# Performance work log

Measured on AMD Instinct MI355X. Metric: run time of the kernel, lower is better.

## Reference

```python
import jax, jax.numpy as jnp
import numpy as np

IN_F, OUT_F = 512, 512
GRID_SIZE, SPLINE_ORDER = 5, 3
K = GRID_SIZE + SPLINE_ORDER  # 8 basis functions
B, S = 8, 1024


def setup_inputs() -> dict:
    key = jax.random.key(0)
    k1, k2, k3, k4, k5 = jax.random.split(key, 5)
    return {
        "x": jax.random.normal(k1, (B, S, IN_F), dtype=jnp.float32),
        "coeff": jax.random.normal(k2, (OUT_F, IN_F, K), dtype=jnp.float32),
        "scale_base": jax.random.normal(k3, (OUT_F, IN_F), dtype=jnp.float32) * 0.1,
        "scale_spline": jax.random.normal(k4, (OUT_F, IN_F), dtype=jnp.float32),
        "base_bias": jax.random.normal(k5, (OUT_F, IN_F), dtype=jnp.float32),
    }


def reference(x, coeff, scale_base, scale_spline, base_bias):
    batch = x.shape[0]
    in_f = x.shape[-1]
    k = coeff.shape[-1]

    xc = jnp.clip(x.reshape(-1, in_f), -1.0, 1.0)      # (N, in)
    base = jax.nn.silu(xc)                              # (N, in)

    # polynomial basis recurrence: b0 = 1, b1 = x, b_i = 2*x*b_{i-1} - 1
    bases = [jnp.ones_like(xc), xc]
    for _ in range(2, k):
        bases.append(2.0 * xc * bases[-1] - 1.0)
    basis = jnp.stack(bases[:k], axis=-1)               # (N, in, K)

    # spline[n,o] = sum_{i,k} scale_spline[o,i]*coeff[o,i,k]*basis[n,i,k]
    w_spline = scale_spline[..., None] * coeff          # (out, in, K)
    spline_term = jnp.einsum('nik,oik->no', basis, w_spline)
    base_term = base @ scale_base.T                     # (N, out)
    out = base_term + spline_term + jnp.sum(base_bias, axis=1)  # (N, out)

    out = out.reshape(batch, -1, base_bias.shape[0])    # (B, S, out)
    if out.shape[-2] == 1:
        out = out[..., 0, :]
    return out
```

## Files before the change

### kernel.cpp

```cpp
#include <hip/hip_runtime.h>
#include <hip/hip_bf16.h>

#define IN_FEAT 512
#define OUT_FEAT 512
#define NTOK 8192
#define KDIM 4096

typedef short bf16x8 __attribute__((ext_vector_type(8)));
typedef float f32x16 __attribute__((ext_vector_type(16)));

static __device__ inline short f2bf(float f) {
    union { float f; unsigned u; } v; v.f = f;
    unsigned u = v.u;
    u += 0x7fffu + ((u >> 16) & 1u);
    return (short)(u >> 16);
}

static __device__ inline unsigned pack2bf(float f0, float f1) {
    union { float f; unsigned u; } a, b; a.f = f0; b.f = f1;
    return __builtin_amdgcn_perm(b.u + 0x8000u, a.u + 0x8000u, 0x07060302u);
}

static __device__ inline bf16x8 gen_chunk(float xv) {
    float xc = fminf(fmaxf(xv, -1.f), 1.f);
    float e  = __expf(-xc);
    float bse = xc * __builtin_amdgcn_rcpf(1.f + e);
    float b2 = 2.f * xc * xc - 1.f;
    float b3 = 2.f * xc * b2 - 1.f;
    float b4 = 2.f * xc * b3 - 1.f;
    float b5 = 2.f * xc * b4 - 1.f;
    float b6 = 2.f * xc * b5 - 1.f;
    float b7 = 2.f * xc * b6 - 1.f;
    union { uint4 u; bf16x8 v; } r;
    r.u.x = pack2bf(bse, xc);
    r.u.y = pack2bf(b2, b3);
    r.u.z = pack2bf(b4, b5);
    r.u.w = pack2bf(b6, b7);
    return r.v;
}

static __device__ inline void gload_lds16(const short* g, short* l) {
    __builtin_amdgcn_global_load_lds(
        (const __attribute__((address_space(1))) unsigned int*)g,
        (__attribute__((address_space(3))) unsigned int*)l,
        16, 0, 0);
}

__global__ __launch_bounds__(256) void kan_prep(
    const float* __restrict__ coeff, const float* __restrict__ scale_base,
    const float* __restrict__ scale_spline, const float* __restrict__ base_bias,
    short* __restrict__ Wb, float* __restrict__ bias)
{
    int o = blockIdx.x;
    int tid = threadIdx.x;
    float local = 0.f;
#pragma unroll
    for (int rep = 0; rep < 2; ++rep) {
        int i = tid + rep * 256;
        size_t oi = (size_t)o * IN_FEAT + i;
        const float4* c4 = (const float4*)(coeff + oi * 8);
        float4 ca = c4[0], cb = c4[1];
        float ss = scale_spline[oi];
        float sb = scale_base[oi];
        local += base_bias[oi] + ss * ca.x;
        bf16x8 w;
        w[0] = f2bf(sb);
        w[1] = f2bf(ss * ca.y); w[2] = f2bf(ss * ca.z); w[3] = f2bf(ss * ca.w);
        w[4] = f2bf(ss * cb.x); w[5] = f2bf(ss * cb.y); w[6] = f2bf(ss * cb.z);
        w[7] = f2bf(ss * cb.w);
        *(bf16x8*)(Wb + (size_t)o * KDIM + (size_t)i * 8) = w;
    }
    __shared__ float red[4];
    for (int off = 32; off > 0; off >>= 1) local += __shfl_down(local, off, 64);
    int lane = tid & 63, wv = tid >> 6;
    if (lane == 0) red[wv] = local;
    __syncthreads();
    if (tid == 0) bias[o] = red[0] + red[1] + red[2] + red[3];
}

__global__ __launch_bounds__(256, 4) void kan_gemm13(
    const float* __restrict__ x, const short* __restrict__ Wb,
    const float* __restrict__ bias, float* __restrict__ out)
{
    __shared__ __align__(16) short POOL[20480];
    short* Bs  = POOL;
    float* xsl = (float*)(POOL + 16384);

    int tid = threadIdx.x;
    int nb = blockIdx.x & 7;
    int mb = blockIdx.x >> 3;
    int m0 = mb * 64, o0 = nb * 64;

    int lane = tid & 63, wv = tid >> 6;
    int kk = wv;
    int l31 = lane & 31, half = lane >> 5;
    int rm  = l31 & 15;
    int xr0 = l31 ^ (kk * 8);

    f32x16 acc[2][2];
#pragma unroll
    for (int a = 0; a < 2; ++a)
#pragma unroll
        for (int b = 0; b < 2; ++b) acc[a][b] = (f32x16)0.f;

    int rl = lane >> 4, q = lane & 15;
    const short* pB0 = Wb + (size_t)(o0 + wv * 16 +  0 + rl) * KDIM + (size_t)(q ^ ( 0 + rl)) * 8;
    const short* pB1 = Wb + (size_t)(o0 + wv * 16 +  4 + rl) * KDIM + (size_t)(q ^ ( 4 + rl)) * 8;
    const short* pB2 = Wb + (size_t)(o0 + wv * 16 +  8 + rl) * KDIM + (size_t)(q ^ ( 8 + rl)) * 8;
    const short* pB3 = Wb + (size_t)(o0 + wv * 16 + 12 + rl) * KDIM + (size_t)(q ^ (12 + rl)) * 8;

    int xrow = tid >> 2, p = tid & 3;
    const float* xg = x + (size_t)(m0 + xrow) * IN_FEAT + p * 4;
    int xb = p * 256 + (xrow ^ (p * 8));

#define STAGE(buf, it)                                                        \
    {                                                                         \
        short* bd_ = Bs + (buf) * 8192 + wv * 2048;                           \
        gload_lds16(pB0 + (size_t)(it) * 128, bd_);                           \
        gload_lds16(pB1 + (size_t)(it) * 128, bd_ + 512);                     \
        gload_lds16(pB2 + (size_t)(it) * 128, bd_ + 1024);                    \
        gload_lds16(pB3 + (size_t)(it) * 128, bd_ + 1536);                    \
        float4 v_ = *(const float4*)(xg + (size_t)(it) * 16);                 \
        float* xd_ = xsl + (buf) * 1024 + xb;                                 \
        xd_[0]   = v_.x;                                                      \
        xd_[64]  = v_.y;                                                      \
        xd_[128] = v_.z;                                                      \
        xd_[192] = v_.w;                                                      \
    }

    STAGE(0, 0);
    int cur = 0;
    for (int it = 0; it < 32; ++it, cur ^= 1) {
        __syncthreads();
        if (it < 31) { int nxt = cur ^ 1; STAGE(nxt, it + 1); }
        const short* Bsc = Bs + cur * 8192;
        const float* xc_ = xsl + cur * 1024;
#pragma unroll
        for (int istep = 0; istep < 2; ++istep) {
            int s = kk * 4 + istep * 2 + half;
            bf16x8 af0 = gen_chunk(xc_[s * 64 + xr0]);
            bf16x8 af1 = gen_chunk(xc_[s * 64 + 32 + xr0]);
            int ph = (s ^ rm) * 8;
            bf16x8 b0 = *(const bf16x8*)(Bsc + l31 * 128 + ph);
            bf16x8 b1 = *(const bf16x8*)(Bsc + (32 + l31) * 128 + ph);
            acc[0][0] = __builtin_amdgcn_mfma_f32_32x32x16_bf16(af0, b0, acc[0][0], 0, 0, 0);
            acc[0][1] = __builtin_amdgcn_mfma_f32_32x32x16_bf16(af0, b1, acc[0][1], 0, 0, 0);
            acc[1][0] = __builtin_amdgcn_mfma_f32_32x32x16_bf16(af1, b0, acc[1][0], 0, 0, 0);
            acc[1][1] = __builtin_amdgcn_mfma_f32_32x32x16_bf16(af1, b1, acc[1][1], 0, 0, 0);
        }
    }
#undef STAGE

    float* rbuf = (float*)POOL;
    __syncthreads();
    if (kk >= 2) {
        float* s_ = rbuf + (size_t)(kk - 2) * 4224 + lane * 66;
#pragma unroll
        for (int fm = 0; fm < 2; ++fm)
#pragma unroll
            for (int fn = 0; fn < 2; ++fn)
#pragma unroll
                for (int r = 0; r < 16; ++r)
                    s_[(fm * 2 + fn) * 16 + r] = acc[fm][fn][r];
    }
    __syncthreads();
    if (kk < 2) {
        const float* s_ = rbuf + (size_t)kk * 4224 + lane * 66;
#pragma unroll
        for (int fm = 0; fm < 2; ++fm)
#pragma unroll
            for (int fn = 0; fn < 2; ++fn)
#pragma unroll
                for (int r = 0; r < 16; ++r)
                    acc[fm][fn][r] += s_[(fm * 2 + fn) * 16 + r];
    }
    __syncthreads();
    if (kk == 1) {
        float* s_ = rbuf + lane * 66;
#pragma unroll
        for (int fm = 0; fm < 2; ++fm)
#pragma unroll
            for (int fn = 0; fn < 2; ++fn)
#pragma unroll
                for (int r = 0; r < 16; ++r)
                    s_[(fm * 2 + fn) * 16 + r] = acc[fm][fn][r];
    }
    __syncthreads();
    if (kk == 0) {
        const float* s_ = rbuf + lane * 66;
#pragma unroll
        for (int fn = 0; fn < 2; ++fn) {
            int o = o0 + fn * 32 + l31;
            float bv = bias[o];
#pragma unroll
            for (int fm = 0; fm < 2; ++fm) {
#pragma unroll
                for (int r = 0; r < 16; ++r) {
                    float v = acc[fm][fn][r] + s_[(fm * 2 + fn) * 16 + r] + bv;
                    int token = m0 + fm * 32 + (r & 3) + 8 * (r >> 2) + 4 * half;
                    out[(size_t)token * OUT_FEAT + o] = v;
                }
            }
        }
    }
}

extern "C" void kernel_launch(void* const* d_in, const int* in_sizes, int n_in,
                              void* d_out, int out_size, void* d_ws, size_t ws_size,
                              hipStream_t stream) {
    const float* x            = (const float*)d_in[0];
    const float* coeff        = (const float*)d_in[1];
    const float* scale_base   = (const float*)d_in[2];
    const float* scale_spline = (const float*)d_in[3];
    const float* base_bias    = (const float*)d_in[4];
    float* out = (float*)d_out;

    short* Wb   = (short*)d_ws;
    float* bias = (float*)((char*)d_ws + (size_t)OUT_FEAT * KDIM * 2);

    kan_prep<<<OUT_FEAT, 256, 0, stream>>>(coeff, scale_base, scale_spline, base_bias, Wb, bias);
    kan_gemm13<<<(NTOK / 64) * (OUT_FEAT / 64), 256, 0, stream>>>(x, Wb, bias, out);
}
```

Measured before the change: 137.7 us.

## Load x directly to registers and hand-schedule GEMM pipeline with explicit waitcnts

The x tile no longer goes through LDS: each lane loads the float4 values it needs straight from global memory into a register double buffer one iteration ahead. The main loop is manually unrolled with sched_barriers, explicit vmcnt/lgkmcnt waits and a raw s_barrier in place of __syncthreads, and MFMA issue runs at raised priority via s_setprio. The aim is to remove the LDS round trip and a full barrier's worth of waiting for x, and to overlap the next tile's loads with MFMA work. In exchange, the launch-bounds occupancy hint drops from 4 to 3 blocks, and correctness now depends on the hand-counted waitcnt values.

```diff
diff --git a/kernel.cpp b/kernel.cpp
--- a/kernel.cpp
+++ b/kernel.cpp
@@ -78,13 +78,12 @@
     if (tid == 0) bias[o] = red[0] + red[1] + red[2] + red[3];
 }
 
-__global__ __launch_bounds__(256, 4) void kan_gemm13(
+__global__ __launch_bounds__(256, 3) void kan_gemm14(
     const float* __restrict__ x, const short* __restrict__ Wb,
     const float* __restrict__ bias, float* __restrict__ out)
 {
     __shared__ __align__(16) short POOL[20480];
-    short* Bs  = POOL;
-    float* xsl = (float*)(POOL + 16384);
+    short* Bs = POOL;
 
     int tid = threadIdx.x;
     int nb = blockIdx.x & 7;
@@ -95,7 +94,6 @@
     int kk = wv;
     int l31 = lane & 31, half = lane >> 5;
     int rm  = l31 & 15;
-    int xr0 = l31 ^ (kk * 8);
 
     f32x16 acc[2][2];
 #pragma unroll
@@ -109,47 +107,90 @@
     const short* pB2 = Wb + (size_t)(o0 + wv * 16 +  8 + rl) * KDIM + (size_t)(q ^ ( 8 + rl)) * 8;
     const short* pB3 = Wb + (size_t)(o0 + wv * 16 + 12 + rl) * KDIM + (size_t)(q ^ (12 + rl)) * 8;
 
-    int xrow = tid >> 2, p = tid & 3;
-    const float* xg = x + (size_t)(m0 + xrow) * IN_FEAT + p * 4;
-    int xb = p * 256 + (xrow ^ (p * 8));
-
-#define STAGE(buf, it)                                                        \
+    const float* xp0 = x + (size_t)(m0 + l31) * IN_FEAT + kk * 4;
+
+    int s0 = kk * 4 + half, s1 = s0 + 2;
+    int of00 = l31 * 128        + ((s0 ^ rm) * 8);
+    int of01 = (32 + l31) * 128 + ((s0 ^ rm) * 8);
+    int of10 = l31 * 128        + ((s1 ^ rm) * 8);
+    int of11 = (32 + l31) * 128 + ((s1 ^ rm) * 8);
+
+#define COMPUTE(CUR, P0, P1)                                                  \
     {                                                                         \
-        short* bd_ = Bs + (buf) * 8192 + wv * 2048;                           \
-        gload_lds16(pB0 + (size_t)(it) * 128, bd_);                           \
-        gload_lds16(pB1 + (size_t)(it) * 128, bd_ + 512);                     \
-        gload_lds16(pB2 + (size_t)(it) * 128, bd_ + 1024);                    \
-        gload_lds16(pB3 + (size_t)(it) * 128, bd_ + 1536);                    \
-        float4 v_ = *(const float4*)(xg + (size_t)(it) * 16);                 \
-        float* xd_ = xsl + (buf) * 1024 + xb;                                 \
-        xd_[0]   = v_.x;                                                      \
-        xd_[64]  = v_.y;                                                      \
-        xd_[128] = v_.z;                                                      \
-        xd_[192] = v_.w;                                                      \
-    }
-
-    STAGE(0, 0);
-    int cur = 0;
-    for (int it = 0; it < 32; ++it, cur ^= 1) {
-        __syncthreads();
-        if (it < 31) { int nxt = cur ^ 1; STAGE(nxt, it + 1); }
-        const short* Bsc = Bs + cur * 8192;
-        const float* xc_ = xsl + cur * 1024;
-#pragma unroll
-        for (int istep = 0; istep < 2; ++istep) {
-            int s = kk * 4 + istep * 2 + half;
-            bf16x8 af0 = gen_chunk(xc_[s * 64 + xr0]);
-            bf16x8 af1 = gen_chunk(xc_[s * 64 + 32 + xr0]);
-            int ph = (s ^ rm) * 8;
-            bf16x8 b0 = *(const bf16x8*)(Bsc + l31 * 128 + ph);
-            bf16x8 b1 = *(const bf16x8*)(Bsc + (32 + l31) * 128 + ph);
-            acc[0][0] = __builtin_amdgcn_mfma_f32_32x32x16_bf16(af0, b0, acc[0][0], 0, 0, 0);
-            acc[0][1] = __builtin_amdgcn_mfma_f32_32x32x16_bf16(af0, b1, acc[0][1], 0, 0, 0);
-            acc[1][0] = __builtin_amdgcn_mfma_f32_32x32x16_bf16(af1, b0, acc[1][0], 0, 0, 0);
-            acc[1][1] = __builtin_amdgcn_mfma_f32_32x32x16_bf16(af1, b1, acc[1][1], 0, 0, 0);
-        }
-    }
-#undef STAGE
+        const short* Bsc_ = Bs + (CUR) * 8192;                                \
+        bf16x8 b00 = *(const bf16x8*)(Bsc_ + of00);                           \
+        bf16x8 b01 = *(const bf16x8*)(Bsc_ + of01);                           \
+        bf16x8 b10 = *(const bf16x8*)(Bsc_ + of10);                           \
+        bf16x8 b11 = *(const bf16x8*)(Bsc_ + of11);                           \
+        bf16x8 a00 = gen_chunk(half ? (P0).y : (P0).x);                       \
+        bf16x8 a01 = gen_chunk(half ? (P1).y : (P1).x);                       \
+        bf16x8 a10 = gen_chunk(half ? (P0).w : (P0).z);                       \
+        bf16x8 a11 = gen_chunk(half ? (P1).w : (P1).z);                       \
+        __builtin_amdgcn_s_setprio(1);                                        \
+        acc[0][0] = __builtin_amdgcn_mfma_f32_32x32x16_bf16(a00, b00, acc[0][0], 0, 0, 0); \
+        acc[0][1] = __builtin_amdgcn_mfma_f32_32x32x16_bf16(a00, b01, acc[0][1], 0, 0, 0); \
+        acc[1][0] = __builtin_amdgcn_mfma_f32_32x32x16_bf16(a01, b00, acc[1][0], 0, 0, 0); \
+        acc[1][1] = __builtin_amdgcn_mfma_f32_32x32x16_bf16(a01, b01, acc[1][1], 0, 0, 0); \
+        acc[0][0] = __builtin_amdgcn_mfma_f32_32x32x16_bf16(a10, b10, acc[0][0], 0, 0, 0); \
+        acc[0][1] = __builtin_amdgcn_mfma_f32_32x32x16_bf16(a10, b11, acc[0][1], 0, 0, 0); \
+        acc[1][0] = __builtin_amdgcn_mfma_f32_32x32x16_bf16(a11, b10, acc[1][0], 0, 0, 0); \
+        acc[1][1] = __builtin_amdgcn_mfma_f32_32x32x16_bf16(a11, b11, acc[1][1], 0, 0, 0); \
+        __builtin_amdgcn_s_setprio(0);                                        \
+    }
+
+#define ITER(IT, CUR, PC0, PC1, PN0, PN1)                                     \
+    {                                                                         \
+        short* bd_ = Bs + ((CUR) ^ 1) * 8192 + wv * 2048;                     \
+        const size_t bo_ = (size_t)((IT) + 1) * 128;                          \
+        gload_lds16(pB0 + bo_, bd_);                                          \
+        gload_lds16(pB1 + bo_, bd_ + 512);                                    \
+        gload_lds16(pB2 + bo_, bd_ + 1024);                                   \
+        gload_lds16(pB3 + bo_, bd_ + 1536);                                   \
+        __builtin_amdgcn_sched_barrier(0);                                    \
+        asm volatile("" ::: "memory");                                        \
+        {                                                                     \
+            const float* xq_ = xp0 + (size_t)((IT) + 1) * 16;                 \
+            PN0 = *(const float4*)(xq_);                                      \
+            PN1 = *(const float4*)(xq_ + 16384);                              \
+        }                                                                     \
+        __builtin_amdgcn_sched_barrier(0);                                    \
+        asm volatile("s_waitcnt vmcnt(6)" ::: "memory");                      \
+        __builtin_amdgcn_sched_barrier(0);                                    \
+        COMPUTE(CUR, PC0, PC1);                                               \
+        asm volatile("s_waitcnt vmcnt(2) lgkmcnt(0)" ::: "memory");           \
+        __builtin_amdgcn_s_barrier();                                         \
+        asm volatile("" ::: "memory");                                        \
+    }
+
+    float4 Pa0, Pa1, Pb0, Pb1;
+
+    {
+        short* bd_ = Bs + wv * 2048;
+        gload_lds16(pB0, bd_);
+        gload_lds16(pB1, bd_ + 512);
+        gload_lds16(pB2, bd_ + 1024);
+        gload_lds16(pB3, bd_ + 1536);
+        __builtin_amdgcn_sched_barrier(0);
+        asm volatile("" ::: "memory");
+        Pa0 = *(const float4*)(xp0);
+        Pa1 = *(const float4*)(xp0 + 16384);
+        __builtin_amdgcn_sched_barrier(0);
+        asm volatile("s_waitcnt vmcnt(2)" ::: "memory");
+        __builtin_amdgcn_s_barrier();
+        asm volatile("" ::: "memory");
+    }
+
+    for (int j = 0; j < 15; ++j) {
+        ITER(2 * j,     0, Pa0, Pa1, Pb0, Pb1);
+        ITER(2 * j + 1, 1, Pb0, Pb1, Pa0, Pa1);
+    }
+    ITER(30, 0, Pa0, Pa1, Pb0, Pb1);
+
+    asm volatile("s_waitcnt vmcnt(0)" ::: "memory");
+    __builtin_amdgcn_sched_barrier(0);
+    COMPUTE(1, Pb0, Pb1);
+#undef ITER
+#undef COMPUTE
 
     float* rbuf = (float*)POOL;
     __syncthreads();
@@ -219,5 +260,5 @@
     float* bias = (float*)((char*)d_ws + (size_t)OUT_FEAT * KDIM * 2);
 
     kan_prep<<<OUT_FEAT, 256, 0, stream>>>(coeff, scale_base, scale_spline, base_bias, Wb, bias);
-    kan_gemm13<<<(NTOK / 64) * (OUT_FEAT / 64), 256, 0, stream>>>(x, Wb, bias, out);
-}
+    kan_gemm14<<<(NTOK / 64) * (OUT_FEAT / 64), 256, 0, stream>>>(x, Wb, bias, out);
+}
```

After: 146.7 us. +6.5%, slower.
